# Kernel tuning notes

Measured on AMD Instinct MI355X. Metric: run time of the kernel, lower is better.

Reference implementation:

```python
import jax, jax.numpy as jnp
import numpy as np

H = 16
D_MODEL = 1024
BLOCK_SIZE = 64
B, S = 2, 2048
NEG = -65504.0  # value used by the torch module for masking


def setup_inputs() -> dict:
    key = jax.random.key(0)
    ks = jax.random.split(key, 12)
    scale = 1.0 / np.sqrt(D_MODEL)
    inp = {
        "query": jax.random.normal(ks[0], (B, S, D_MODEL), jnp.float32),
        "key": jax.random.normal(ks[1], (B, S, D_MODEL), jnp.float32),
        "value": jax.random.normal(ks[2], (B, S, D_MODEL), jnp.float32),
        "Wq": jax.random.normal(ks[3], (D_MODEL, D_MODEL), jnp.float32) * scale,
        "bq": jnp.zeros((D_MODEL,), jnp.float32),
        "Wk": jax.random.normal(ks[4], (D_MODEL, D_MODEL), jnp.float32) * scale,
        "bk": jnp.zeros((D_MODEL,), jnp.float32),
        "Wv": jax.random.normal(ks[5], (D_MODEL, D_MODEL), jnp.float32) * scale,
        "bv": jnp.zeros((D_MODEL,), jnp.float32),
        "Wo": jax.random.normal(ks[6], (D_MODEL, D_MODEL), jnp.float32) * scale,
        "bo": jnp.zeros((D_MODEL,), jnp.float32),
    }
    return inp


def reference(query, key, value, Wq, bq, Wk, bk, Wv, bv, Wo, bo):
    b, s, d = query.shape
    dk = d // H

    def proj(x, W, bias):
        # [b,s,d] -> [b,h,s,dk]
        return (x @ W + bias).reshape(b, s, H, dk).transpose(0, 2, 1, 3)

    q = proj(query, Wq, bq)
    k = proj(key, Wk, bk)
    v = proj(value, Wv, bv)

    # dense QK^T / sqrt(d_k), exactly as the torch module (then block mask added)
    scores = jnp.einsum("bhqd,bhkd->bhqk", q, k) / jnp.sqrt(jnp.float32(dk))

    bid = jnp.arange(s) // BLOCK_SIZE
    attn_mask = jnp.where(bid[:, None] == bid[None, :], 0.0, NEG).astype(scores.dtype)
    scores = scores + attn_mask  # broadcast over [b,h]

    attn = jax.nn.softmax(scores, axis=-1)
    x = jnp.einsum("bhqk,bhkd->bhqd", attn, v)
    x = x.transpose(0, 2, 1, 3).reshape(b, s, d)
    return x @ Wo + bo
```

## Files before the change

kernel.cpp:

```cpp
#include <hip/hip_runtime.h>
#include <hip/hip_bf16.h>

typedef __attribute__((ext_vector_type(4))) float f32x4;
typedef __attribute__((ext_vector_type(8))) short s16x8;

#define MFMA16(a, b, c) __builtin_amdgcn_mfma_f32_16x16x32_bf16(a, b, c, 0, 0, 0)

__device__ __forceinline__ void gld_lds16(const void* g, void* l) {
  __builtin_amdgcn_global_load_lds(
      (const __attribute__((address_space(1))) unsigned int*)g,
      (__attribute__((address_space(3))) unsigned int*)l, 16, 0, 0);
}

__device__ __forceinline__ unsigned short f2bf(float f) {
  union { __hip_bfloat16 b; unsigned short u; } cv;
  cv.b = __float2bfloat16(f);
  return cv.u;
}
__device__ __forceinline__ float bf2f(unsigned short u) {
  union { unsigned short u; __hip_bfloat16 b; } cv;
  cv.u = u;
  return __bfloat162float(cv.b);
}

__global__ void transw(const float* W0, unsigned short* H0,
                       const float* W1, unsigned short* H1,
                       const float* W2, unsigned short* H2,
                       const float* W3, unsigned short* H3) {
  __shared__ float tile[64 * 65];
  const float* W; unsigned short* H;
  switch (blockIdx.y) {
    case 0: W = W0; H = H0; break;
    case 1: W = W1; H = H1; break;
    case 2: W = W2; H = H2; break;
    default: W = W3; H = H3; break;
  }
  const int t = threadIdx.x;
  const int tk0 = (blockIdx.x & 15) * 64;
  const int tn0 = (blockIdx.x >> 4) * 64;
  for (int i = 0; i < 16; ++i) {
    int idx = i * 256 + t;
    int r = idx >> 6, c = idx & 63;
    tile[r * 65 + c] = W[(size_t)(tk0 + r) * 1024 + tn0 + c];
  }
  __syncthreads();
  for (int i = 0; i < 16; ++i) {
    int idx = i * 256 + t;
    int r = idx >> 6, c = idx & 63;
    H[(size_t)(tn0 + r) * 1024 + tk0 + c] = f2bf(tile[c * 65 + r]);
  }
}

__global__ void convert_x3(const float* A0, unsigned short* H0,
                           const float* A1, unsigned short* H1,
                           const float* A2, unsigned short* H2) {
  const float* src; unsigned short* h;
  switch (blockIdx.y) {
    case 0: src = A0; h = H0; break;
    case 1: src = A1; h = H1; break;
    default: src = A2; h = H2; break;
  }
  int i = blockIdx.x * 256 + threadIdx.x;
  float4 v = ((const float4*)src)[i];
  ((ushort4*)h)[i] = make_ushort4(f2bf(v.x), f2bf(v.y), f2bf(v.z), f2bf(v.w));
}


struct QkvArgs {
  const unsigned short* A[3];
  const unsigned short* B[3];
  const float* bias[3];
  unsigned short* out[3];
};

__global__ __launch_bounds__(512, 2)
void gemm_qkv(QkvArgs args) {
  const int K = 1024;
  __shared__ __align__(16) unsigned short lds[65536];
  const int tid = threadIdx.x;
  const int lane = tid & 63, w = tid >> 6;

  const int nwg = 192;
  const int orig = blockIdx.x;
  const int swz = (orig & 7) * (nwg >> 3) + (orig >> 3);
  const int g = swz >> 6;
  const int tl = swz & 63;
  const int m0 = (tl >> 2) * 256, n0 = (tl & 3) * 256;

  const unsigned short* A = args.A[g];
  const unsigned short* B = args.B[g];
  const float* bias = args.bias[g];
  unsigned short* out = args.out[g];

  const int wm = (w >> 2) * 128, wn = (w & 3) * 64;
  const int fr = lane & 15, gh = lane >> 4;

  const unsigned short* aP[4]; const unsigned short* bP[4]; int dstoff[4];
  #pragma unroll
  for (int s = 0; s < 4; ++s) {
    const int G = s * 512 + tid;
    const int r = G >> 3, slot = G & 7;
    const int gno = slot ^ (r & 7);
    const int ko = (gno >> 2) * 32 + (gno & 3) * 8;
    aP[s] = A + (size_t)(m0 + r) * K + ko;
    bP[s] = B + (size_t)(n0 + r) * K + ko;
    dstoff[s] = G * 8;
  }
  auto stageAll = [&](int u, int kt) {
    #pragma unroll
    for (int s = 0; s < 4; ++s) {
      gld_lds16(aP[s] + kt, &lds[u * 16384 + dstoff[s]]);
      gld_lds16(bP[s] + kt, &lds[32768 + u * 16384 + dstoff[s]]);
    }
  };

  f32x4 acc[8][4] = {};

  stageAll(0, 0);
  asm volatile("s_waitcnt vmcnt(0)" ::: "memory");
  __builtin_amdgcn_s_barrier();
  __builtin_amdgcn_sched_barrier(0);

  #pragma unroll 1
  for (int t = 0; t < 16; ++t) {
    const int u = t & 1;
    if (t < 15) stageAll(u ^ 1, (t + 1) * 64);
    const unsigned short* La = &lds[u * 16384];
    const unsigned short* Lb = &lds[32768 + u * 16384];
    s16x8 b[2][4];
    #pragma unroll
    for (int ks = 0; ks < 2; ++ks)
      #pragma unroll
      for (int nt = 0; nt < 4; ++nt) {
        const int br = wn + nt * 16 + fr;
        b[ks][nt] = *(const s16x8*)&Lb[br * 64 + (((ks << 2) | gh) ^ (br & 7)) * 8];
      }
    #pragma unroll
    for (int q = 0; q < 4; ++q) {
      s16x8 a[2][2];
      #pragma unroll
      for (int i = 0; i < 2; ++i)
        #pragma unroll
        for (int ks = 0; ks < 2; ++ks) {
          const int ar = wm + (q * 2 + i) * 16 + fr;
          a[i][ks] = *(const s16x8*)&La[ar * 64 + (((ks << 2) | gh) ^ (ar & 7)) * 8];
        }
      #pragma unroll
      for (int i = 0; i < 2; ++i)
        #pragma unroll
        for (int nt = 0; nt < 4; ++nt) {
          acc[q * 2 + i][nt] = MFMA16(a[i][0], b[0][nt], acc[q * 2 + i][nt]);
          acc[q * 2 + i][nt] = MFMA16(a[i][1], b[1][nt], acc[q * 2 + i][nt]);
        }
    }
    __builtin_amdgcn_sched_barrier(0);
    if (t < 15) { asm volatile("s_waitcnt vmcnt(0)" ::: "memory"); }
    __builtin_amdgcn_s_barrier();
    __builtin_amdgcn_sched_barrier(0);
  }

  float bv[4];
  #pragma unroll
  for (int nt = 0; nt < 4; ++nt) bv[nt] = bias[n0 + wn + nt * 16 + fr];
  unsigned short* eb = &lds[0];
  __syncthreads();
  if (g == 2) {
    #pragma unroll
    for (int mt = 0; mt < 8; ++mt)
      #pragma unroll
      for (int nt = 0; nt < 4; ++nt) {
        const int nl = wn + nt * 16 + fr;
        f32x4 r = acc[mt][nt];
        #pragma unroll
        for (int j = 0; j < 4; ++j) {
          const int sl = wm + mt * 16 + gh * 4 + j;
          eb[sl * 256 + (nl ^ ((sl >> 3) & 31))] = f2bf(r[j] + bv[nt]);
        }
      }
  } else {
    #pragma unroll
    for (int mt = 0; mt < 8; ++mt)
      #pragma unroll
      for (int nt = 0; nt < 4; ++nt) {
        const int nl = wn + nt * 16 + fr;
        f32x4 r = acc[mt][nt];
        #pragma unroll
        for (int j = 0; j < 4; ++j) {
          const int sl = wm + mt * 16 + gh * 4 + j;
          eb[sl * 256 + nl] = f2bf(r[j] + bv[nt]);
        }
      }
  }
  __syncthreads();
  const int b2 = m0 >> 11;
  if (g == 2) {
    #pragma unroll
    for (int it = 0; it < 16; ++it) {
      const int u = it * 512 + tid;
      const int nl = u >> 5, sc = u & 31;
      s16x8 v;
      #pragma unroll
      for (int r = 0; r < 8; ++r)
        v[r] = (short)eb[(sc * 8 + r) * 256 + (nl ^ sc)];
      const int gn = n0 + nl, h = gn >> 6, d = gn & 63;
      *(s16x8*)&out[((size_t)((b2 * 16 + h) * 64 + d)) * 2048 + (m0 & 2047) + sc * 8] = v;
    }
  } else {
    #pragma unroll
    for (int it = 0; it < 16; ++it) {
      const int u = it * 512 + tid;
      const int sl = u >> 5, n8 = (u & 31) * 8;
      s16x8 v = *(const s16x8*)&eb[sl * 256 + n8];
      const int s = m0 + sl;
      const int gn = n0 + n8, h = gn >> 6, d = gn & 63;
      *(s16x8*)&out[(((size_t)(b2 * 16 + h)) * 2048 + (s & 2047)) * 64 + d] = v;
    }
  }
}

__global__ __launch_bounds__(256, 2)
void gemm_oproj(const unsigned short* __restrict__ A, const unsigned short* __restrict__ B,
                const float* __restrict__ bias, float* __restrict__ out) {
  const int K = 1024, N = 1024;
  __shared__ __align__(16) unsigned short lds[32768];
  const int tid = threadIdx.x;
  const int lane = tid & 63, wid = tid >> 6;

  const int nwg = 256;
  const int orig = blockIdx.x;
  const int swz = (orig & 7) * (nwg >> 3) + (orig >> 3);
  const int m0 = (swz >> 3) * 128, n0 = (swz & 7) * 128;

  const int wm = (wid >> 1) * 64, wn = (wid & 1) * 64;
  const int fr = lane & 15, gh = lane >> 4;

  const unsigned short* aP[4]; const unsigned short* bP[4]; int dstoff[4];
  #pragma unroll
  for (int s = 0; s < 4; ++s) {
    const int G = s * 256 + tid;
    const int r = G >> 3, slot = G & 7;
    const int gno = slot ^ (r & 7);
    const int ko = (gno >> 2) * 32 + (gno & 3) * 8;
    aP[s] = A + (size_t)(m0 + r) * K + ko;
    bP[s] = B + (size_t)(n0 + r) * K + ko;
    dstoff[s] = G * 8;
  }
  auto stageAll = [&](int u, int kt) {
    #pragma unroll
    for (int s = 0; s < 4; ++s) {
      gld_lds16(aP[s] + kt, &lds[u * 8192 + dstoff[s]]);
      gld_lds16(bP[s] + kt, &lds[16384 + u * 8192 + dstoff[s]]);
    }
  };

  f32x4 acc[4][4] = {};

  stageAll(0, 0);
  asm volatile("s_waitcnt vmcnt(0)" ::: "memory");
  __builtin_amdgcn_s_barrier();
  __builtin_amdgcn_sched_barrier(0);

  #pragma unroll 1
  for (int t = 0; t < 16; ++t) {
    const int u = t & 1;
    if (t < 15) stageAll(u ^ 1, (t + 1) * 64);
    const unsigned short* La = &lds[u * 8192];
    const unsigned short* Lb = &lds[16384 + u * 8192];
    s16x8 b[2][4];
    #pragma unroll
    for (int ks = 0; ks < 2; ++ks)
      #pragma unroll
      for (int nt = 0; nt < 4; ++nt) {
        const int br = wn + nt * 16 + fr;
        b[ks][nt] = *(const s16x8*)&Lb[br * 64 + (((ks << 2) | gh) ^ (br & 7)) * 8];
      }
    #pragma unroll
    for (int q = 0; q < 2; ++q) {
      s16x8 a[2][2];
      #pragma unroll
      for (int i = 0; i < 2; ++i)
        #pragma unroll
        for (int ks = 0; ks < 2; ++ks) {
          const int ar = wm + (q * 2 + i) * 16 + fr;
          a[i][ks] = *(const s16x8*)&La[ar * 64 + (((ks << 2) | gh) ^ (ar & 7)) * 8];
        }
      #pragma unroll
      for (int i = 0; i < 2; ++i)
        #pragma unroll
        for (int nt = 0; nt < 4; ++nt) {
          acc[q * 2 + i][nt] = MFMA16(a[i][0], b[0][nt], acc[q * 2 + i][nt]);
          acc[q * 2 + i][nt] = MFMA16(a[i][1], b[1][nt], acc[q * 2 + i][nt]);
        }
    }
    __builtin_amdgcn_sched_barrier(0);
    if (t < 15) { asm volatile("s_waitcnt vmcnt(0)" ::: "memory"); }
    __builtin_amdgcn_s_barrier();
    __builtin_amdgcn_sched_barrier(0);
  }

  #pragma unroll
  for (int mt = 0; mt < 4; ++mt) {
    const int gm = m0 + wm + mt * 16 + (gh << 2);
    #pragma unroll
    for (int nt = 0; nt < 4; ++nt) {
      const int gn = n0 + wn + nt * 16 + fr;
      const float bvv = bias[gn];
      f32x4 r = acc[mt][nt];
      #pragma unroll
      for (int j = 0; j < 4; ++j)
        out[(size_t)(gm + j) * N + gn] = r[j] + bvv;
    }
  }
}

__global__ __launch_bounds__(256, 2)
void attn_mfma(const unsigned short* __restrict__ Q, const unsigned short* __restrict__ Kb,
               const unsigned short* __restrict__ Vt, unsigned short* __restrict__ X) {
  __shared__ __align__(16) unsigned short qs[4096];
  __shared__ __align__(16) unsigned short ks2[4096];
  __shared__ __align__(16) unsigned short vs[4096];
  __shared__ __align__(16) unsigned short ps[4096];
  const int tid = threadIdx.x, lane = tid & 63, w = tid >> 6;
  const int hb = blockIdx.x >> 5, qb = blockIdx.x & 31;
  const size_t qkbase = ((size_t)hb * 2048 + qb * 64) * 64;
  const size_t vbase = (size_t)hb * 64 * 2048 + qb * 64;

  #pragma unroll
  for (int i = 0; i < 2; ++i) {
    const int G = i * 256 + tid;
    const int row = G >> 3, slot = G & 7;
    const int sg = slot ^ (row & 7);
    gld_lds16(Q + qkbase + row * 64 + sg * 8, &qs[G * 8]);
    gld_lds16(Kb + qkbase + row * 64 + sg * 8, &ks2[G * 8]);
    gld_lds16(Vt + vbase + (size_t)row * 2048 + sg * 8, &vs[G * 8]);
  }
  asm volatile("s_waitcnt vmcnt(0)" ::: "memory");
  __syncthreads();

  const int fr = lane & 15, gh = lane >> 4;
  const int arow = w * 16 + fr;

  s16x8 aq[2], bk[2][4];
  #pragma unroll
  for (int ks = 0; ks < 2; ++ks) {
    aq[ks] = *(const s16x8*)&qs[arow * 64 + (((ks * 4 + gh) ^ (arow & 7)) << 3)];
    #pragma unroll
    for (int nt = 0; nt < 4; ++nt) {
      const int krow = nt * 16 + fr;
      bk[ks][nt] = *(const s16x8*)&ks2[krow * 64 + (((ks * 4 + gh) ^ (krow & 7)) << 3)];
    }
  }
  f32x4 s[4] = {};
  #pragma unroll
  for (int ks = 0; ks < 2; ++ks)
    #pragma unroll
    for (int nt = 0; nt < 4; ++nt)
      s[nt] = MFMA16(aq[ks], bk[ks][nt], s[nt]);

  #pragma unroll
  for (int j = 0; j < 4; ++j) {
    float t0 = s[0][j] * 0.125f, t1 = s[1][j] * 0.125f;
    float t2 = s[2][j] * 0.125f, t3 = s[3][j] * 0.125f;
    float m = fmaxf(fmaxf(t0, t1), fmaxf(t2, t3));
    m = fmaxf(m, __shfl_xor(m, 1, 64));
    m = fmaxf(m, __shfl_xor(m, 2, 64));
    m = fmaxf(m, __shfl_xor(m, 4, 64));
    m = fmaxf(m, __shfl_xor(m, 8, 64));
    t0 = __expf(t0 - m); t1 = __expf(t1 - m);
    t2 = __expf(t2 - m); t3 = __expf(t3 - m);
    float sum = t0 + t1 + t2 + t3;
    sum += __shfl_xor(sum, 1, 64);
    sum += __shfl_xor(sum, 2, 64);
    sum += __shfl_xor(sum, 4, 64);
    sum += __shfl_xor(sum, 8, 64);
    const float r = 1.0f / sum;
    s[0][j] = t0 * r; s[1][j] = t1 * r; s[2][j] = t2 * r; s[3][j] = t3 * r;
  }

  #pragma unroll
  for (int j = 0; j < 4; ++j) {
    const int q = w * 16 + gh * 4 + j;
    #pragma unroll
    for (int nt = 0; nt < 4; ++nt) {
      const int k = nt * 16 + fr;
      ps[q * 64 + (((k >> 3) ^ (q & 7)) << 3) + (k & 7)] = f2bf(s[nt][j]);
    }
  }

  s16x8 ap[2], bv2[2][4];
  #pragma unroll
  for (int ks = 0; ks < 2; ++ks) {
    ap[ks] = *(const s16x8*)&ps[arow * 64 + (((ks * 4 + gh) ^ (arow & 7)) << 3)];
    #pragma unroll
    for (int nt = 0; nt < 4; ++nt) {
      const int drow = nt * 16 + fr;
      bv2[ks][nt] = *(const s16x8*)&vs[drow * 64 + (((ks * 4 + gh) ^ (drow & 7)) << 3)];
    }
  }
  f32x4 x[4] = {};
  #pragma unroll
  for (int ks = 0; ks < 2; ++ks)
    #pragma unroll
    for (int nt = 0; nt < 4; ++nt)
      x[nt] = MFMA16(ap[ks], bv2[ks][nt], x[nt]);

  const int b = hb >> 4, h = hb & 15;
  #pragma unroll
  for (int nt = 0; nt < 4; ++nt)
    #pragma unroll
    for (int j = 0; j < 4; ++j) {
      const int sgl = qb * 64 + w * 16 + gh * 4 + j;
      X[((size_t)(b * 2048 + sgl)) * 1024 + h * 64 + nt * 16 + fr] = f2bf(x[nt][j]);
    }
}

extern "C" void kernel_launch(void* const* d_in, const int* in_sizes, int n_in,
                              void* d_out, int out_size, void* d_ws, size_t ws_size,
                              hipStream_t stream) {
  const float* query = (const float*)d_in[0];
  const float* key   = (const float*)d_in[1];
  const float* value = (const float*)d_in[2];
  const float* Wq = (const float*)d_in[3]; const float* bq = (const float*)d_in[4];
  const float* Wk = (const float*)d_in[5]; const float* bk = (const float*)d_in[6];
  const float* Wv = (const float*)d_in[7]; const float* bv = (const float*)d_in[8];
  const float* Wo = (const float*)d_in[9]; const float* bo = (const float*)d_in[10];
  float* out = (float*)d_out;

  const size_t W_E = 1024 * 1024;
  const size_t X_E = 4096 * 1024;
  unsigned char* p = (unsigned char*)d_ws;
  auto take = [&](size_t bytes) { void* r = (void*)p; p += bytes; return r; };

  unsigned short* wtq = (unsigned short*)take(W_E * 2);
  unsigned short* wtk = (unsigned short*)take(W_E * 2);
  unsigned short* wtv = (unsigned short*)take(W_E * 2);
  unsigned short* wto = (unsigned short*)take(W_E * 2);
  unsigned short* xq = (unsigned short*)take(X_E * 2);
  unsigned short* xk = (unsigned short*)take(X_E * 2);
  unsigned short* xv = (unsigned short*)take(X_E * 2);
  unsigned short* Qb = (unsigned short*)take(X_E * 2);
  unsigned short* Kb = (unsigned short*)take(X_E * 2);
  unsigned short* Vt = (unsigned short*)take(X_E * 2);
  unsigned short* ao = (unsigned short*)take(X_E * 2);
  (void)ws_size; (void)in_sizes; (void)n_in; (void)out_size;

  transw<<<dim3(256, 4), 256, 0, stream>>>(Wq, wtq, Wk, wtk, Wv, wtv, Wo, wto);
  convert_x3<<<dim3(4096, 3), 256, 0, stream>>>(query, xq, key, xk, value, xv);

  QkvArgs qkv = {};
  qkv.A[0] = xq; qkv.B[0] = wtq; qkv.bias[0] = bq; qkv.out[0] = Qb;
  qkv.A[1] = xk; qkv.B[1] = wtk; qkv.bias[1] = bk; qkv.out[1] = Kb;
  qkv.A[2] = xv; qkv.B[2] = wtv; qkv.bias[2] = bv; qkv.out[2] = Vt;
  gemm_qkv<<<dim3(192), 512, 0, stream>>>(qkv);

  attn_mfma<<<dim3(1024), 256, 0, stream>>>(Qb, Kb, Vt, ao);

  gemm_oproj<<<dim3(256), 256, 0, stream>>>(ao, wto, bo, out);
}
```

Before: 78.93 us.

## Fuse fp32-to-bf16 activation conversion into QKV GEMM A-tile staging

Removes the separate convert_x3 kernel. The QKV GEMM now loads fp32 query/key/value rows into registers, converts them to bf16, and writes them into swizzled LDS. The global load is issued before the MFMA work and the LDS write is deferred until after it, so the load latency overlaps compute. This saves one launch plus the bf16 round trip through global memory, at the cost of extra registers and VALU conversion work inside the GEMM loop. The V-transpose epilogue also changes its LDS swizzle so it can use vectorized 16-byte reads instead of eight scalar reads.

```diff
diff --git a/kernel.cpp b/kernel.cpp
--- a/kernel.cpp
+++ b/kernel.cpp
@@ -51,23 +51,9 @@
   }
 }
 
-__global__ void convert_x3(const float* A0, unsigned short* H0,
-                           const float* A1, unsigned short* H1,
-                           const float* A2, unsigned short* H2) {
-  const float* src; unsigned short* h;
-  switch (blockIdx.y) {
-    case 0: src = A0; h = H0; break;
-    case 1: src = A1; h = H1; break;
-    default: src = A2; h = H2; break;
-  }
-  int i = blockIdx.x * 256 + threadIdx.x;
-  float4 v = ((const float4*)src)[i];
-  ((ushort4*)h)[i] = make_ushort4(f2bf(v.x), f2bf(v.y), f2bf(v.z), f2bf(v.w));
-}
-
 
 struct QkvArgs {
-  const unsigned short* A[3];
+  const float* A[3];
   const unsigned short* B[3];
   const float* bias[3];
   unsigned short* out[3];
@@ -87,7 +73,7 @@
   const int tl = swz & 63;
   const int m0 = (tl >> 2) * 256, n0 = (tl & 3) * 256;
 
-  const unsigned short* A = args.A[g];
+  const float* A = args.A[g];
   const unsigned short* B = args.B[g];
   const float* bias = args.bias[g];
   unsigned short* out = args.out[g];
@@ -95,36 +81,67 @@
   const int wm = (w >> 2) * 128, wn = (w & 3) * 64;
   const int fr = lane & 15, gh = lane >> 4;
 
-  const unsigned short* aP[4]; const unsigned short* bP[4]; int dstoff[4];
+  const int ar_ = tid >> 1;
+  const int p_ = tid & 1;
+  const int khalf = p_ ^ ((ar_ >> 2) & 1);
+  const float* aSrc = A + (size_t)(m0 + ar_) * K + khalf * 32;
+
+  const unsigned short* bP[4]; int bDst[4];
   #pragma unroll
   for (int s = 0; s < 4; ++s) {
     const int G = s * 512 + tid;
     const int r = G >> 3, slot = G & 7;
     const int gno = slot ^ (r & 7);
     const int ko = (gno >> 2) * 32 + (gno & 3) * 8;
-    aP[s] = A + (size_t)(m0 + r) * K + ko;
     bP[s] = B + (size_t)(n0 + r) * K + ko;
-    dstoff[s] = G * 8;
-  }
-  auto stageAll = [&](int u, int kt) {
-    #pragma unroll
-    for (int s = 0; s < 4; ++s) {
-      gld_lds16(aP[s] + kt, &lds[u * 16384 + dstoff[s]]);
-      gld_lds16(bP[s] + kt, &lds[32768 + u * 16384 + dstoff[s]]);
-    }
+    bDst[s] = G * 8;
+  }
+  auto stageB = [&](int u, int kt) {
+    #pragma unroll
+    for (int s = 0; s < 4; ++s)
+      gld_lds16(bP[s] + kt, &lds[32768 + u * 16384 + bDst[s]]);
   };
 
+  float4 av[8];
+  auto loadA = [&](int kt) {
+    #pragma unroll
+    for (int j = 0; j < 8; ++j)
+      av[j] = *(const float4*)(aSrc + kt + j * 4);
+  };
+  auto writeA = [&](int u) {
+    #pragma unroll
+    for (int j = 0; j < 4; ++j) {
+      const float4 lo = av[2 * j], hi = av[2 * j + 1];
+      s16x8 v;
+      v[0] = (short)f2bf(lo.x); v[1] = (short)f2bf(lo.y);
+      v[2] = (short)f2bf(lo.z); v[3] = (short)f2bf(lo.w);
+      v[4] = (short)f2bf(hi.x); v[5] = (short)f2bf(hi.y);
+      v[6] = (short)f2bf(hi.z); v[7] = (short)f2bf(hi.w);
+      const int slot = (khalf * 4 + j) ^ (ar_ & 7);
+      *(s16x8*)&lds[u * 16384 + ar_ * 64 + slot * 8] = v;
+    }
+  };
+
   f32x4 acc[8][4] = {};
 
-  stageAll(0, 0);
-  asm volatile("s_waitcnt vmcnt(0)" ::: "memory");
+  loadA(0);
+  stageB(0, 0);
+  asm volatile("s_waitcnt vmcnt(4)" ::: "memory");
+  writeA(0);
+  asm volatile("s_waitcnt vmcnt(0) lgkmcnt(0)" ::: "memory");
   __builtin_amdgcn_s_barrier();
   __builtin_amdgcn_sched_barrier(0);
 
   #pragma unroll 1
   for (int t = 0; t < 16; ++t) {
     const int u = t & 1;
-    if (t < 15) stageAll(u ^ 1, (t + 1) * 64);
+    if (t < 15) {
+      loadA((t + 1) * 64);
+      stageB(u ^ 1, (t + 1) * 64);
+      asm volatile("s_waitcnt vmcnt(12)" ::: "memory");
+    } else {
+      asm volatile("s_waitcnt vmcnt(0)" ::: "memory");
+    }
     const unsigned short* La = &lds[u * 16384];
     const unsigned short* Lb = &lds[32768 + u * 16384];
     s16x8 b[2][4];
@@ -153,8 +170,12 @@
           acc[q * 2 + i][nt] = MFMA16(a[i][1], b[1][nt], acc[q * 2 + i][nt]);
         }
     }
+    if (t < 15) {
+      asm volatile("s_waitcnt vmcnt(4)" ::: "memory");
+      writeA(u ^ 1);
+      asm volatile("s_waitcnt lgkmcnt(0)" ::: "memory");
+    }
     __builtin_amdgcn_sched_barrier(0);
-    if (t < 15) { asm volatile("s_waitcnt vmcnt(0)" ::: "memory"); }
     __builtin_amdgcn_s_barrier();
     __builtin_amdgcn_sched_barrier(0);
   }
@@ -174,7 +195,7 @@
         #pragma unroll
         for (int j = 0; j < 4; ++j) {
           const int sl = wm + mt * 16 + gh * 4 + j;
-          eb[sl * 256 + (nl ^ ((sl >> 3) & 31))] = f2bf(r[j] + bv[nt]);
+          eb[nl * 256 + (sl ^ ((nl & 7) << 3))] = f2bf(r[j] + bv[nt]);
         }
       }
   } else {
@@ -198,10 +219,7 @@
     for (int it = 0; it < 16; ++it) {
       const int u = it * 512 + tid;
       const int nl = u >> 5, sc = u & 31;
-      s16x8 v;
-      #pragma unroll
-      for (int r = 0; r < 8; ++r)
-        v[r] = (short)eb[(sc * 8 + r) * 256 + (nl ^ sc)];
+      s16x8 v = *(const s16x8*)&eb[nl * 256 + ((sc * 8) ^ ((nl & 7) << 3))];
       const int gn = n0 + nl, h = gn >> 6, d = gn & 63;
       *(s16x8*)&out[((size_t)((b2 * 16 + h) * 64 + d)) * 2048 + (m0 & 2047) + sc * 8] = v;
     }
@@ -435,9 +453,6 @@
   unsigned short* wtk = (unsigned short*)take(W_E * 2);
   unsigned short* wtv = (unsigned short*)take(W_E * 2);
   unsigned short* wto = (unsigned short*)take(W_E * 2);
-  unsigned short* xq = (unsigned short*)take(X_E * 2);
-  unsigned short* xk = (unsigned short*)take(X_E * 2);
-  unsigned short* xv = (unsigned short*)take(X_E * 2);
   unsigned short* Qb = (unsigned short*)take(X_E * 2);
   unsigned short* Kb = (unsigned short*)take(X_E * 2);
   unsigned short* Vt = (unsigned short*)take(X_E * 2);
@@ -445,12 +460,11 @@
   (void)ws_size; (void)in_sizes; (void)n_in; (void)out_size;
 
   transw<<<dim3(256, 4), 256, 0, stream>>>(Wq, wtq, Wk, wtk, Wv, wtv, Wo, wto);
-  convert_x3<<<dim3(4096, 3), 256, 0, stream>>>(query, xq, key, xk, value, xv);
 
   QkvArgs qkv = {};
-  qkv.A[0] = xq; qkv.B[0] = wtq; qkv.bias[0] = bq; qkv.out[0] = Qb;
-  qkv.A[1] = xk; qkv.B[1] = wtk; qkv.bias[1] = bk; qkv.out[1] = Kb;
-  qkv.A[2] = xv; qkv.B[2] = wtv; qkv.bias[2] = bv; qkv.out[2] = Vt;
+  qkv.A[0] = query; qkv.B[0] = wtq; qkv.bias[0] = bq; qkv.out[0] = Qb;
+  qkv.A[1] = key;   qkv.B[1] = wtk; qkv.bias[1] = bk; qkv.out[1] = Kb;
+  qkv.A[2] = value; qkv.B[2] = wtv; qkv.bias[2] = bv; qkv.out[2] = Vt;
   gemm_qkv<<<dim3(192), 512, 0, stream>>>(qkv);
 
   attn_mfma<<<dim3(1024), 256, 0, stream>>>(Qb, Kb, Vt, ao);
```

Measured after the change: 90.48 us. 1.15x slower.

## Interleave staged global loads with MFMA phases and transpose V epilogue in LDS

Applied to the files above, without the earlier changes.

Splits each K-tile of the fused QKV projection GEMM into four phases. Each phase loads a 32-row slice of A fragments, issues part of the next tile's global-to-LDS copies, and then runs MFMAs at raised wave priority, with partial vmcnt waits in place of a full drain. This is meant to overlap memory traffic with matrix work instead of loading everything and waiting at the end of each tile. Separately, the transposed V epilogue now stores into LDS in transposed, XOR-swizzled order, so the readback is one vector load instead of eight scalar gathers. The added barriers per tile and the hand-tuned wait counts add sync overhead and fragility.

```diff
diff --git a/kernel.cpp b/kernel.cpp
--- a/kernel.cpp
+++ b/kernel.cpp
@@ -95,66 +95,151 @@
   const int wm = (w >> 2) * 128, wn = (w & 3) * 64;
   const int fr = lane & 15, gh = lane >> 4;
 
-  const unsigned short* aP[4]; const unsigned short* bP[4]; int dstoff[4];
-  #pragma unroll
-  for (int s = 0; s < 4; ++s) {
-    const int G = s * 512 + tid;
-    const int r = G >> 3, slot = G & 7;
+  const unsigned short* bSrc[2][2]; int bDst[2][2];
+  #pragma unroll
+  for (int g2 = 0; g2 < 2; ++g2)
+    #pragma unroll
+    for (int i = 0; i < 2; ++i) {
+      const int G = i * 512 + tid;
+      const int lr = G >> 3, slot = G & 7;
+      const int r = g2 * 128 + lr;
+      const int gno = slot ^ (r & 7);
+      const int ko = (gno >> 2) * 32 + (gno & 3) * 8;
+      bSrc[g2][i] = B + (size_t)(n0 + r) * K + ko;
+      bDst[g2][i] = r * 64 + slot * 8;
+    }
+  const unsigned short* aSrc[4]; int aDst[4];
+  #pragma unroll
+  for (int p = 0; p < 4; ++p) {
+    const int lr = tid >> 3, slot = tid & 7;
+    const int r = ((lr >> 5) << 7) + p * 32 + (lr & 31);
     const int gno = slot ^ (r & 7);
     const int ko = (gno >> 2) * 32 + (gno & 3) * 8;
-    aP[s] = A + (size_t)(m0 + r) * K + ko;
-    bP[s] = B + (size_t)(n0 + r) * K + ko;
-    dstoff[s] = G * 8;
-  }
-  auto stageAll = [&](int u, int kt) {
-    #pragma unroll
-    for (int s = 0; s < 4; ++s) {
-      gld_lds16(aP[s] + kt, &lds[u * 16384 + dstoff[s]]);
-      gld_lds16(bP[s] + kt, &lds[32768 + u * 16384 + dstoff[s]]);
-    }
+    aSrc[p] = A + (size_t)(m0 + r) * K + ko;
+    aDst[p] = r * 64 + slot * 8;
+  }
+
+  auto stageB = [&](int u, int g2, int kt) {
+    gld_lds16(bSrc[g2][0] + kt, &lds[32768 + u * 16384 + bDst[g2][0]]);
+    gld_lds16(bSrc[g2][1] + kt, &lds[32768 + u * 16384 + bDst[g2][1]]);
   };
+  auto stageA2 = [&](int u, int pp, int kt) {
+    gld_lds16(aSrc[pp] + kt, &lds[u * 16384 + aDst[pp]]);
+    gld_lds16(aSrc[pp + 1] + kt, &lds[u * 16384 + aDst[pp + 1]]);
+  };
 
   f32x4 acc[8][4] = {};
 
-  stageAll(0, 0);
-  asm volatile("s_waitcnt vmcnt(0)" ::: "memory");
+  stageB(0, 0, 0); stageB(0, 1, 0); stageA2(0, 0, 0); stageA2(0, 2, 0);
+  asm volatile("s_waitcnt vmcnt(2)" ::: "memory");
   __builtin_amdgcn_s_barrier();
   __builtin_amdgcn_sched_barrier(0);
 
   #pragma unroll 1
   for (int t = 0; t < 16; ++t) {
     const int u = t & 1;
-    if (t < 15) stageAll(u ^ 1, (t + 1) * 64);
     const unsigned short* La = &lds[u * 16384];
     const unsigned short* Lb = &lds[32768 + u * 16384];
-    s16x8 b[2][4];
+    const int nkt = (t + 1) * 64;
+    s16x8 breg[2][4];
+    s16x8 a[2][2];
+
     #pragma unroll
     for (int ks = 0; ks < 2; ++ks)
       #pragma unroll
       for (int nt = 0; nt < 4; ++nt) {
         const int br = wn + nt * 16 + fr;
-        b[ks][nt] = *(const s16x8*)&Lb[br * 64 + (((ks << 2) | gh) ^ (br & 7)) * 8];
-      }
-    #pragma unroll
-    for (int q = 0; q < 4; ++q) {
-      s16x8 a[2][2];
-      #pragma unroll
-      for (int i = 0; i < 2; ++i)
-        #pragma unroll
-        for (int ks = 0; ks < 2; ++ks) {
-          const int ar = wm + (q * 2 + i) * 16 + fr;
-          a[i][ks] = *(const s16x8*)&La[ar * 64 + (((ks << 2) | gh) ^ (ar & 7)) * 8];
-        }
-      #pragma unroll
-      for (int i = 0; i < 2; ++i)
-        #pragma unroll
-        for (int nt = 0; nt < 4; ++nt) {
-          acc[q * 2 + i][nt] = MFMA16(a[i][0], b[0][nt], acc[q * 2 + i][nt]);
-          acc[q * 2 + i][nt] = MFMA16(a[i][1], b[1][nt], acc[q * 2 + i][nt]);
-        }
-    }
-    __builtin_amdgcn_sched_barrier(0);
-    if (t < 15) { asm volatile("s_waitcnt vmcnt(0)" ::: "memory"); }
+        breg[ks][nt] = *(const s16x8*)&Lb[br * 64 + (((ks << 2) | gh) ^ (br & 7)) * 8];
+      }
+    #pragma unroll
+    for (int i = 0; i < 2; ++i)
+      #pragma unroll
+      for (int ks = 0; ks < 2; ++ks) {
+        const int ar = wm + i * 16 + fr;
+        a[i][ks] = *(const s16x8*)&La[ar * 64 + (((ks << 2) | gh) ^ (ar & 7)) * 8];
+      }
+    if (t < 15) stageB(u ^ 1, 0, nkt);
+    __builtin_amdgcn_s_barrier();
+    asm volatile("s_waitcnt lgkmcnt(0)" ::: "memory");
+    __builtin_amdgcn_sched_barrier(0);
+    __builtin_amdgcn_s_setprio(1);
+    #pragma unroll
+    for (int i = 0; i < 2; ++i)
+      #pragma unroll
+      for (int nt = 0; nt < 4; ++nt) {
+        acc[i][nt] = MFMA16(a[i][0], breg[0][nt], acc[i][nt]);
+        acc[i][nt] = MFMA16(a[i][1], breg[1][nt], acc[i][nt]);
+      }
+    __builtin_amdgcn_s_setprio(0);
+    __builtin_amdgcn_s_barrier();
+
+    #pragma unroll
+    for (int i = 0; i < 2; ++i)
+      #pragma unroll
+      for (int ks = 0; ks < 2; ++ks) {
+        const int ar = wm + 32 + i * 16 + fr;
+        a[i][ks] = *(const s16x8*)&La[ar * 64 + (((ks << 2) | gh) ^ (ar & 7)) * 8];
+      }
+    if (t < 15) stageB(u ^ 1, 1, nkt);
+    __builtin_amdgcn_s_barrier();
+    asm volatile("s_waitcnt lgkmcnt(0)" ::: "memory");
+    __builtin_amdgcn_sched_barrier(0);
+    __builtin_amdgcn_s_setprio(1);
+    #pragma unroll
+    for (int i = 0; i < 2; ++i)
+      #pragma unroll
+      for (int nt = 0; nt < 4; ++nt) {
+        acc[2 + i][nt] = MFMA16(a[i][0], breg[0][nt], acc[2 + i][nt]);
+        acc[2 + i][nt] = MFMA16(a[i][1], breg[1][nt], acc[2 + i][nt]);
+      }
+    __builtin_amdgcn_s_setprio(0);
+    if (t < 15) { asm volatile("s_waitcnt vmcnt(4)" ::: "memory"); }
+    else        { asm volatile("s_waitcnt vmcnt(0)" ::: "memory"); }
+    __builtin_amdgcn_s_barrier();
+
+    #pragma unroll
+    for (int i = 0; i < 2; ++i)
+      #pragma unroll
+      for (int ks = 0; ks < 2; ++ks) {
+        const int ar = wm + 64 + i * 16 + fr;
+        a[i][ks] = *(const s16x8*)&La[ar * 64 + (((ks << 2) | gh) ^ (ar & 7)) * 8];
+      }
+    if (t < 15) stageA2(u ^ 1, 0, nkt);
+    __builtin_amdgcn_s_barrier();
+    asm volatile("s_waitcnt lgkmcnt(0)" ::: "memory");
+    __builtin_amdgcn_sched_barrier(0);
+    __builtin_amdgcn_s_setprio(1);
+    #pragma unroll
+    for (int i = 0; i < 2; ++i)
+      #pragma unroll
+      for (int nt = 0; nt < 4; ++nt) {
+        acc[4 + i][nt] = MFMA16(a[i][0], breg[0][nt], acc[4 + i][nt]);
+        acc[4 + i][nt] = MFMA16(a[i][1], breg[1][nt], acc[4 + i][nt]);
+      }
+    __builtin_amdgcn_s_setprio(0);
+    __builtin_amdgcn_s_barrier();
+
+    #pragma unroll
+    for (int i = 0; i < 2; ++i)
+      #pragma unroll
+      for (int ks = 0; ks < 2; ++ks) {
+        const int ar = wm + 96 + i * 16 + fr;
+        a[i][ks] = *(const s16x8*)&La[ar * 64 + (((ks << 2) | gh) ^ (ar & 7)) * 8];
+      }
+    if (t < 15) stageA2(u ^ 1, 2, nkt);
+    __builtin_amdgcn_s_barrier();
+    asm volatile("s_waitcnt lgkmcnt(0)" ::: "memory");
+    __builtin_amdgcn_sched_barrier(0);
+    __builtin_amdgcn_s_setprio(1);
+    #pragma unroll
+    for (int i = 0; i < 2; ++i)
+      #pragma unroll
+      for (int nt = 0; nt < 4; ++nt) {
+        acc[6 + i][nt] = MFMA16(a[i][0], breg[0][nt], acc[6 + i][nt]);
+        acc[6 + i][nt] = MFMA16(a[i][1], breg[1][nt], acc[6 + i][nt]);
+      }
+    __builtin_amdgcn_s_setprio(0);
+    asm volatile("s_waitcnt vmcnt(2)" ::: "memory");
     __builtin_amdgcn_s_barrier();
     __builtin_amdgcn_sched_barrier(0);
   }
@@ -174,7 +259,7 @@
         #pragma unroll
         for (int j = 0; j < 4; ++j) {
           const int sl = wm + mt * 16 + gh * 4 + j;
-          eb[sl * 256 + (nl ^ ((sl >> 3) & 31))] = f2bf(r[j] + bv[nt]);
+          eb[nl * 256 + (sl ^ ((nl & 7) << 3))] = f2bf(r[j] + bv[nt]);
         }
       }
   } else {
@@ -198,10 +283,7 @@
     for (int it = 0; it < 16; ++it) {
       const int u = it * 512 + tid;
       const int nl = u >> 5, sc = u & 31;
-      s16x8 v;
-      #pragma unroll
-      for (int r = 0; r < 8; ++r)
-        v[r] = (short)eb[(sc * 8 + r) * 256 + (nl ^ sc)];
+      s16x8 v = *(const s16x8*)&eb[nl * 256 + ((sc * 8) ^ ((nl & 7) << 3))];
       const int gn = n0 + nl, h = gn >> 6, d = gn & 63;
       *(s16x8*)&out[((size_t)((b2 * 16 + h) * 64 + d)) * 2048 + (m0 & 2047) + sc * 8] = v;
     }
```

After: 80.95 us. 2.6% more time.

## Merge prep kernels, vectorize V-transpose epilogue, overlap V load in attention

Applied to the files above, without the earlier changes.

Combines the weight transpose and activation conversion kernels into one launch to cut a kernel launch and its tail. Changes the transposed LDS staging for the V output in the QKV GEMM so each thread reads 8 contiguous bf16 values with one vector load instead of 8 scalar reads, using an XOR swizzle. In attention, issues the V loads last and waits only for Q/K before QK^T, deferring the V wait until before the PV matmul so the V fetch overlaps with the score and softmax work. The partial vmcnt wait depends on how the compiler orders and counts the outstanding loads.

```diff
diff --git a/kernel.cpp b/kernel.cpp
--- a/kernel.cpp
+++ b/kernel.cpp
@@ -23,46 +23,49 @@
   return __bfloat162float(cv.b);
 }
 
-__global__ void transw(const float* W0, unsigned short* H0,
-                       const float* W1, unsigned short* H1,
-                       const float* W2, unsigned short* H2,
-                       const float* W3, unsigned short* H3) {
+__global__ void prep(const float* Xq, unsigned short* xq,
+                     const float* Xk, unsigned short* xk,
+                     const float* Xv, unsigned short* xv,
+                     const float* W0, unsigned short* H0,
+                     const float* W1, unsigned short* H1,
+                     const float* W2, unsigned short* H2,
+                     const float* W3, unsigned short* H3) {
   __shared__ float tile[64 * 65];
-  const float* W; unsigned short* H;
-  switch (blockIdx.y) {
-    case 0: W = W0; H = H0; break;
-    case 1: W = W1; H = H1; break;
-    case 2: W = W2; H = H2; break;
-    default: W = W3; H = H3; break;
-  }
+  const int bid = blockIdx.x;
   const int t = threadIdx.x;
-  const int tk0 = (blockIdx.x & 15) * 64;
-  const int tn0 = (blockIdx.x >> 4) * 64;
-  for (int i = 0; i < 16; ++i) {
-    int idx = i * 256 + t;
-    int r = idx >> 6, c = idx & 63;
-    tile[r * 65 + c] = W[(size_t)(tk0 + r) * 1024 + tn0 + c];
-  }
-  __syncthreads();
-  for (int i = 0; i < 16; ++i) {
-    int idx = i * 256 + t;
-    int r = idx >> 6, c = idx & 63;
-    H[(size_t)(tn0 + r) * 1024 + tk0 + c] = f2bf(tile[c * 65 + r]);
-  }
-}
-
-__global__ void convert_x3(const float* A0, unsigned short* H0,
-                           const float* A1, unsigned short* H1,
-                           const float* A2, unsigned short* H2) {
-  const float* src; unsigned short* h;
-  switch (blockIdx.y) {
-    case 0: src = A0; h = H0; break;
-    case 1: src = A1; h = H1; break;
-    default: src = A2; h = H2; break;
-  }
-  int i = blockIdx.x * 256 + threadIdx.x;
-  float4 v = ((const float4*)src)[i];
-  ((ushort4*)h)[i] = make_ushort4(f2bf(v.x), f2bf(v.y), f2bf(v.z), f2bf(v.w));
+  if (bid < 12288) {
+    const float* src; unsigned short* h;
+    const int which = bid / 4096;
+    if (which == 0) { src = Xq; h = xq; }
+    else if (which == 1) { src = Xk; h = xk; }
+    else { src = Xv; h = xv; }
+    const int i = (bid - which * 4096) * 256 + t;
+    float4 v = ((const float4*)src)[i];
+    ((ushort4*)h)[i] = make_ushort4(f2bf(v.x), f2bf(v.y), f2bf(v.z), f2bf(v.w));
+  } else {
+    const int bid2 = bid - 12288;
+    const float* W; unsigned short* H;
+    switch (bid2 >> 8) {
+      case 0: W = W0; H = H0; break;
+      case 1: W = W1; H = H1; break;
+      case 2: W = W2; H = H2; break;
+      default: W = W3; H = H3; break;
+    }
+    const int tx = bid2 & 255;
+    const int tk0 = (tx & 15) * 64;
+    const int tn0 = (tx >> 4) * 64;
+    for (int i = 0; i < 16; ++i) {
+      int idx = i * 256 + t;
+      int r = idx >> 6, c = idx & 63;
+      tile[r * 65 + c] = W[(size_t)(tk0 + r) * 1024 + tn0 + c];
+    }
+    __syncthreads();
+    for (int i = 0; i < 16; ++i) {
+      int idx = i * 256 + t;
+      int r = idx >> 6, c = idx & 63;
+      H[(size_t)(tn0 + r) * 1024 + tk0 + c] = f2bf(tile[c * 65 + r]);
+    }
+  }
 }
 
 
@@ -174,7 +177,7 @@
         #pragma unroll
         for (int j = 0; j < 4; ++j) {
           const int sl = wm + mt * 16 + gh * 4 + j;
-          eb[sl * 256 + (nl ^ ((sl >> 3) & 31))] = f2bf(r[j] + bv[nt]);
+          eb[nl * 256 + (sl ^ ((nl & 7) << 3))] = f2bf(r[j] + bv[nt]);
         }
       }
   } else {
@@ -198,10 +201,7 @@
     for (int it = 0; it < 16; ++it) {
       const int u = it * 512 + tid;
       const int nl = u >> 5, sc = u & 31;
-      s16x8 v;
-      #pragma unroll
-      for (int r = 0; r < 8; ++r)
-        v[r] = (short)eb[(sc * 8 + r) * 256 + (nl ^ sc)];
+      s16x8 v = *(const s16x8*)&eb[nl * 256 + ((sc * 8) ^ ((nl & 7) << 3))];
       const int gn = n0 + nl, h = gn >> 6, d = gn & 63;
       *(s16x8*)&out[((size_t)((b2 * 16 + h) * 64 + d)) * 2048 + (m0 & 2047) + sc * 8] = v;
     }
@@ -332,10 +332,17 @@
     const int sg = slot ^ (row & 7);
     gld_lds16(Q + qkbase + row * 64 + sg * 8, &qs[G * 8]);
     gld_lds16(Kb + qkbase + row * 64 + sg * 8, &ks2[G * 8]);
+  }
+  #pragma unroll
+  for (int i = 0; i < 2; ++i) {
+    const int G = i * 256 + tid;
+    const int row = G >> 3, slot = G & 7;
+    const int sg = slot ^ (row & 7);
     gld_lds16(Vt + vbase + (size_t)row * 2048 + sg * 8, &vs[G * 8]);
   }
-  asm volatile("s_waitcnt vmcnt(0)" ::: "memory");
-  __syncthreads();
+  asm volatile("s_waitcnt vmcnt(2)" ::: "memory");
+  __builtin_amdgcn_s_barrier();
+  __builtin_amdgcn_sched_barrier(0);
 
   const int fr = lane & 15, gh = lane >> 4;
   const int arow = w * 16 + fr;
@@ -387,6 +394,10 @@
     }
   }
 
+  asm volatile("s_waitcnt vmcnt(0)" ::: "memory");
+  __builtin_amdgcn_s_barrier();
+  __builtin_amdgcn_sched_barrier(0);
+
   s16x8 ap[2], bv2[2][4];
   #pragma unroll
   for (int ks = 0; ks < 2; ++ks) {
@@ -444,8 +455,8 @@
   unsigned short* ao = (unsigned short*)take(X_E * 2);
   (void)ws_size; (void)in_sizes; (void)n_in; (void)out_size;
 
-  transw<<<dim3(256, 4), 256, 0, stream>>>(Wq, wtq, Wk, wtk, Wv, wtv, Wo, wto);
-  convert_x3<<<dim3(4096, 3), 256, 0, stream>>>(query, xq, key, xk, value, xv);
+  prep<<<dim3(13312), 256, 0, stream>>>(query, xq, key, xk, value, xv,
+                                        Wq, wtq, Wk, wtk, Wv, wtv, Wo, wto);
 
   QkvArgs qkv = {};
   qkv.A[0] = xq; qkv.B[0] = wtq; qkv.bias[0] = bq; qkv.out[0] = Qb;
```

Result: faster. 76.96 us (-2.5%).
